# Performance work log

Measured on AMD Instinct MI355X. Metric: run time of the kernel, lower is better.

Reference implementation:

```python
import jax, jax.numpy as jnp
import numpy as np

B, T, A, D = 256, 2048, 22, 2
MAX_GAP = 512  # max NaN-gap length injected per row


def setup_inputs() -> dict:
    key = jax.random.key(0)
    k1, k2, k3 = jax.random.split(key, 3)
    x = jax.random.normal(k1, (B, T, A, D), dtype=jnp.float32)
    # one contiguous NaN gap per row: frames (s, e) exclusive are NaN
    s = jax.random.randint(k2, (B,), 1, T // 2)        # last valid frame before gap
    gap = jax.random.randint(k3, (B,), 1, MAX_GAP)     # gap length
    e = s + gap + 1                                    # first valid frame after gap
    t = jnp.arange(T)
    gap_mask = (t[None, :] > s[:, None]) & (t[None, :] < e[:, None])  # [B, T]
    x = jnp.where(gap_mask[:, :, None, None], jnp.nan, x)
    return {"x": x}


def reference(x):
    # x: [B, T, A, D] with one contiguous NaN gap along T per row.
    Bn, Tn = x.shape[0], x.shape[1]
    nan_mask = jnp.isnan(x).reshape(Bn, Tn, -1).any(axis=2)       # [B, T]
    start = jnp.argmax(nan_mask, axis=1) - 1                       # last valid before gap
    end = Tn - jnp.argmax(nan_mask[:, ::-1], axis=1)               # first valid after gap

    b = jnp.arange(Bn)
    x_s = x[b, start]                                              # [B, A, D]
    x_e = x[b, end]                                                # [B, A, D]

    t = jnp.arange(Tn)[None, :]                                    # [1, T]
    # weight at frame t is (t - s) / (e - s), matching linspace(0,1,gap+2)[1:-1]
    w = (t - start[:, None]).astype(x.dtype) / (end - start)[:, None].astype(x.dtype)
    w = w[:, :, None, None]                                        # [B, T, 1, 1]
    interp = x_s[:, None] * (1.0 - w) + x_e[:, None] * w           # [B, T, A, D]

    in_gap = (t > start[:, None]) & (t < end[:, None])             # [B, T]
    return jnp.where(in_gap[:, :, None, None], interp, x)
```

## Files before the change

### kernel.cpp

```cpp
#include <hip/hip_runtime.h>

#define BB 256
#define TT 2048
#define AD 44
#define AD4 11
#define BLOCKS_PER_B 88

__global__ __launch_bounds__(256) void find_gap_kernel(
    const float* __restrict__ x,
    int* __restrict__ starts,
    int* __restrict__ ends,
    float* __restrict__ xs,
    float* __restrict__ xe) {
  const int b = blockIdx.x;
  const int tid = threadIdx.x;
  const float* row = x + (size_t)b * TT * AD;

  int lmin = TT;
  int lmax = -1;
  for (int t = tid; t < TT; t += 256) {
    float v = row[(size_t)t * AD];
    if (v != v) {
      lmin = min(lmin, t);
      lmax = max(lmax, t);
    }
  }

  __shared__ int smin[256];
  __shared__ int smax[256];
  smin[tid] = lmin;
  smax[tid] = lmax;
  __syncthreads();
  for (int s = 128; s > 0; s >>= 1) {
    if (tid < s) {
      smin[tid] = min(smin[tid], smin[tid + s]);
      smax[tid] = max(smax[tid], smax[tid + s]);
    }
    __syncthreads();
  }

  __shared__ int s_start, s_end;
  if (tid == 0) {
    s_start = smin[0] - 1;
    s_end   = smax[0] + 1;
    starts[b] = s_start;
    ends[b]   = s_end;
  }
  __syncthreads();

  const int st = s_start;
  const int en = s_end;
  if (tid < AD) {
    xs[b * AD + tid] = row[(size_t)st * AD + tid];
    xe[b * AD + tid] = row[(size_t)en * AD + tid];
  }
}

__global__ __launch_bounds__(256) void interp_kernel(
    const float4* __restrict__ x4,
    float4* __restrict__ out4,
    const int* __restrict__ starts,
    const int* __restrict__ ends,
    const float4* __restrict__ xs4,
    const float4* __restrict__ xe4) {
  const int b = blockIdx.x / BLOCKS_PER_B;
  const int rem = (blockIdx.x % BLOCKS_PER_B) * 256 + threadIdx.x;
  const int t = rem / AD4;
  const int c4 = rem - t * AD4;
  const size_t idx = (size_t)b * (TT * AD4) + rem;

  float4 v = x4[idx];
  const int s = starts[b];
  const int e = ends[b];
  if (t > s && t < e) {
    const float w = (float)(t - s) / (float)(e - s);
    const float omw = 1.0f - w;
    const float4 a = xs4[b * AD4 + c4];
    const float4 z = xe4[b * AD4 + c4];
    v.x = a.x * omw + z.x * w;
    v.y = a.y * omw + z.y * w;
    v.z = a.z * omw + z.z * w;
    v.w = a.w * omw + z.w * w;
  }
  out4[idx] = v;
}

extern "C" void kernel_launch(void* const* d_in, const int* in_sizes, int n_in,
                              void* d_out, int out_size, void* d_ws, size_t ws_size,
                              hipStream_t stream) {
  const float* x = (const float*)d_in[0];
  float* out = (float*)d_out;

  char* ws = (char*)d_ws;
  int* starts = (int*)(ws);
  int* ends = (int*)(ws + 1024);
  float* xs = (float*)(ws + 2048);
  float* xe = (float*)(ws + 2048 + BB * AD * sizeof(float));

  find_gap_kernel<<<BB, 256, 0, stream>>>(x, starts, ends, xs, xe);

  interp_kernel<<<BB * BLOCKS_PER_B, 256, 0, stream>>>(
      (const float4*)x, (float4*)out, starts, ends,
      (const float4*)xs, (const float4*)xe);
}
```

Baseline: 169.9 us.

## Fuse NaN-gap detection into streaming copy and patch only gap frames afterward

```diff
diff --git a/kernel.cpp b/kernel.cpp
--- a/kernel.cpp
+++ b/kernel.cpp
@@ -4,102 +4,87 @@
 #define TT 2048
 #define AD 44
 #define AD4 11
-#define BLOCKS_PER_B 88
+#define F4_PER_B (TT * AD4)
+#define NBLK (BB * F4_PER_B / 256)
 
-__global__ __launch_bounds__(256) void find_gap_kernel(
-    const float* __restrict__ x,
-    int* __restrict__ starts,
-    int* __restrict__ ends,
-    float* __restrict__ xs,
-    float* __restrict__ xe) {
-  const int b = blockIdx.x;
-  const int tid = threadIdx.x;
-  const float* row = x + (size_t)b * TT * AD;
+typedef float v4 __attribute__((ext_vector_type(4)));
 
-  int lmin = TT;
-  int lmax = -1;
-  for (int t = tid; t < TT; t += 256) {
-    float v = row[(size_t)t * AD];
-    if (v != v) {
-      lmin = min(lmin, t);
-      lmax = max(lmax, t);
+__global__ __launch_bounds__(256) void init_minmax(unsigned* __restrict__ mn,
+                                                   unsigned* __restrict__ mxk) {
+  mn[threadIdx.x] = 0xFFFFFFFFu;
+  mxk[threadIdx.x] = 0xFFFFFFFFu;
+}
+
+__global__ __launch_bounds__(256) void scan_copy(const v4* __restrict__ x4,
+                                                 v4* __restrict__ out4,
+                                                 unsigned* __restrict__ mn,
+                                                 unsigned* __restrict__ mxk) {
+  const int gid = blockIdx.x * 256 + threadIdx.x;
+  const int b = gid / F4_PER_B;
+  const int rem = gid - b * F4_PER_B;
+  const int t = rem / AD4;
+
+  const v4 v = x4[gid];
+  __builtin_nontemporal_store(v, &out4[gid]);
+
+  const bool n = (v.x != v.x) || (v.y != v.y) || (v.z != v.z) || (v.w != v.w);
+  const unsigned long long m = __ballot(n);
+  if (m != 0ull) {
+    const int fl = __ffsll((unsigned long long)m) - 1;
+    const int ll = 63 - __clzll((unsigned long long)m);
+    const int tmin = __shfl(t, fl);
+    const int tmax = __shfl(t, ll);
+    if ((threadIdx.x & 63) == 0) {
+      atomicMin(&mn[b], (unsigned)tmin);
+      atomicMin(&mxk[b], (unsigned)(4096 - tmax));
     }
-  }
-
-  __shared__ int smin[256];
-  __shared__ int smax[256];
-  smin[tid] = lmin;
-  smax[tid] = lmax;
-  __syncthreads();
-  for (int s = 128; s > 0; s >>= 1) {
-    if (tid < s) {
-      smin[tid] = min(smin[tid], smin[tid + s]);
-      smax[tid] = max(smax[tid], smax[tid + s]);
-    }
-    __syncthreads();
-  }
-
-  __shared__ int s_start, s_end;
-  if (tid == 0) {
-    s_start = smin[0] - 1;
-    s_end   = smax[0] + 1;
-    starts[b] = s_start;
-    ends[b]   = s_end;
-  }
-  __syncthreads();
-
-  const int st = s_start;
-  const int en = s_end;
-  if (tid < AD) {
-    xs[b * AD + tid] = row[(size_t)st * AD + tid];
-    xe[b * AD + tid] = row[(size_t)en * AD + tid];
   }
 }
 
-__global__ __launch_bounds__(256) void interp_kernel(
-    const float4* __restrict__ x4,
-    float4* __restrict__ out4,
-    const int* __restrict__ starts,
-    const int* __restrict__ ends,
-    const float4* __restrict__ xs4,
-    const float4* __restrict__ xe4) {
-  const int b = blockIdx.x / BLOCKS_PER_B;
-  const int rem = (blockIdx.x % BLOCKS_PER_B) * 256 + threadIdx.x;
-  const int t = rem / AD4;
-  const int c4 = rem - t * AD4;
-  const size_t idx = (size_t)b * (TT * AD4) + rem;
+__global__ __launch_bounds__(256) void fix_gap(const v4* __restrict__ x4,
+                                               v4* __restrict__ out4,
+                                               const unsigned* __restrict__ mn,
+                                               const unsigned* __restrict__ mxk) {
+  const int b = blockIdx.x;
+  const int tid = threadIdx.x;
+  const int s = (int)mn[b] - 1;
+  const int e = (4096 - (int)mxk[b]) + 1;
 
-  float4 v = x4[idx];
-  const int s = starts[b];
-  const int e = ends[b];
-  if (t > s && t < e) {
-    const float w = (float)(t - s) / (float)(e - s);
-    const float omw = 1.0f - w;
-    const float4 a = xs4[b * AD4 + c4];
-    const float4 z = xe4[b * AD4 + c4];
-    v.x = a.x * omw + z.x * w;
-    v.y = a.y * omw + z.y * w;
-    v.z = a.z * omw + z.z * w;
-    v.w = a.w * omw + z.w * w;
+  __shared__ v4 sxs[AD4], sxe[AD4];
+  const size_t base = (size_t)b * F4_PER_B;
+  if (tid < AD4) sxs[tid] = x4[base + (size_t)s * AD4 + tid];
+  if (tid >= 64 && tid < 64 + AD4) sxe[tid - 64] = x4[base + (size_t)e * AD4 + (tid - 64)];
+  __syncthreads();
+
+  const float inv = 1.0f / (float)(e - s);
+  const int total = (e - s - 1) * AD4;
+  for (int i = tid; i < total; i += 256) {
+    const int dt = i / AD4;
+    const int c = i - dt * AD4;
+    const int t = s + 1 + dt;
+    const float w = (float)(dt + 1) * inv;
+    const float om = 1.0f - w;
+    const v4 a = sxs[c];
+    const v4 z = sxe[c];
+    v4 r;
+    r.x = a.x * om + z.x * w;
+    r.y = a.y * om + z.y * w;
+    r.z = a.z * om + z.z * w;
+    r.w = a.w * om + z.w * w;
+    __builtin_nontemporal_store(r, &out4[base + (size_t)t * AD4 + c]);
   }
-  out4[idx] = v;
 }
 
 extern "C" void kernel_launch(void* const* d_in, const int* in_sizes, int n_in,
                               void* d_out, int out_size, void* d_ws, size_t ws_size,
                               hipStream_t stream) {
-  const float* x = (const float*)d_in[0];
-  float* out = (float*)d_out;
+  const v4* x4 = (const v4*)d_in[0];
+  v4* out4 = (v4*)d_out;
 
-  char* ws = (char*)d_ws;
-  int* starts = (int*)(ws);
-  int* ends = (int*)(ws + 1024);
-  float* xs = (float*)(ws + 2048);
-  float* xe = (float*)(ws + 2048 + BB * AD * sizeof(float));
+  unsigned* mn = (unsigned*)d_ws;
+  unsigned* mxk = (unsigned*)((char*)d_ws + 1024);
 
-  find_gap_kernel<<<BB, 256, 0, stream>>>(x, starts, ends, xs, xe);
-
-  interp_kernel<<<BB * BLOCKS_PER_B, 256, 0, stream>>>(
-      (const float4*)x, (float4*)out, starts, ends,
-      (const float4*)xs, (const float4*)xe);
+  init_minmax<<<1, 256, 0, stream>>>(mn, mxk);
+  scan_copy<<<NBLK, 256, 0, stream>>>(x4, out4, mn, mxk);
+  fix_gap<<<BB, 256, 0, stream>>>(x4, out4, mn, mxk);
 }
```

Result: slower. 176.9 us (+4.1%).
